# Performance work log

Hardware: AMD Instinct MI355X
Metric: run time of the kernel (lower is better)

The kernel has to match this reference:

```python
import jax, jax.numpy as jnp
import numpy as np

N_ENT = 50000
N_REL = 500
IN_DIM = 128
OUT_DIM = 128
N_EDGES = 500000
LRELU_SLOPE = 0.01  # torch F.leaky_relu default


def setup_inputs() -> dict:
    key = jax.random.key(0)
    ks = jax.random.split(key, 8)
    # triplets [3, E]: row0=src entity, row1=relation, row2=dst entity.
    # Ensure every entity appears as a source so no 0/0 in the edge-softmax division.
    src_extra = jax.random.randint(ks[0], (N_EDGES - N_ENT,), 0, N_ENT)
    src = jnp.concatenate([jnp.arange(N_ENT), src_extra])
    rel = jax.random.randint(ks[1], (N_EDGES,), 0, N_REL)
    dst = jax.random.randint(ks[2], (N_EDGES,), 0, N_ENT)
    triplets = jnp.stack([src, rel, dst]).astype(jnp.int64)
    ent_embed = jax.random.normal(ks[3], (N_ENT, IN_DIM), dtype=jnp.float32)
    rel_embed = jax.random.normal(ks[4], (N_REL, IN_DIM), dtype=jnp.float32)
    adj = jax.random.randint(ks[5], (2, N_EDGES), 0, N_ENT).astype(jnp.int64)  # unused by forward
    # Xavier-normal (gain=1.414) init for the two linear layers, like the torch module.
    std_a = 1.414 * np.sqrt(2.0 / (3 * IN_DIM + OUT_DIM))
    std_a2 = 1.414 * np.sqrt(2.0 / (OUT_DIM + 1))
    W_a = jax.random.normal(ks[6], (3 * IN_DIM, OUT_DIM), dtype=jnp.float32) * std_a
    b_a = jnp.zeros((OUT_DIM,), dtype=jnp.float32)
    W_a2 = jax.random.normal(ks[7], (OUT_DIM, 1), dtype=jnp.float32) * std_a2
    b_a2 = jnp.zeros((1,), dtype=jnp.float32)
    return {"triplets": triplets, "ent_embed": ent_embed, "rel_embed": rel_embed,
            "adj": adj, "W_a": W_a, "b_a": b_a, "W_a2": W_a2, "b_a2": b_a2}


def reference(triplets, ent_embed, rel_embed, adj, W_a, b_a, W_a2, b_a2):
    src, rel, dst = triplets[0], triplets[1], triplets[2]
    n_ent = ent_embed.shape[0]
    # Gather + concat: [E, 3*in_dim]
    h = jnp.concatenate([ent_embed[src], rel_embed[rel], ent_embed[dst]], axis=1)
    c = h @ W_a + b_a                                   # [E, out_dim]
    b = jax.nn.leaky_relu(c @ W_a2 + b_a2, LRELU_SLOPE)  # [E, 1]
    e_b = jnp.exp(b)                                    # [E, 1]
    # Sparse edge-softmax grouped by source node (sparse.sum over dst dim).
    denom = jax.ops.segment_sum(e_b, src, num_segments=n_ent)        # [N, 1]
    numer = jax.ops.segment_sum(e_b * c, src, num_segments=n_ent)    # [N, out_dim]
    out = numer / denom
    return jax.nn.elu(out)  # concat=True branch
```

## Files before the change

kernel.cpp:

```cpp
#include <hip/hip_runtime.h>

#define DIM 128

typedef __attribute__((ext_vector_type(8))) short bf16x8;
typedef __attribute__((ext_vector_type(4))) float f32x4;

__device__ inline unsigned short to_bf16(float f) {
    unsigned u = __float_as_uint(f);
    u = (u + 0x7FFFu + ((u >> 16) & 1u)) >> 16;
    return (unsigned short)u;
}
__device__ inline unsigned pack_bf16(float lo, float hi) {
    return (unsigned)to_bf16(lo) | ((unsigned)to_bf16(hi) << 16);
}
__device__ inline float unpack_lo(unsigned v) { return __uint_as_float(v << 16); }
__device__ inline float unpack_hi(unsigned v) { return __uint_as_float(v & 0xFFFF0000u); }

__global__ void wprep_kernel(const float* __restrict__ W_a, unsigned short* __restrict__ Wt,
                             int* __restrict__ counts, int n) {
    const int c = blockIdx.x;
    const int k = threadIdx.x;
    const int srow = (c < 128) ? k : (256 + k);
    const int scol = (c < 128) ? c : (c - 128);
    Wt[c * DIM + k] = to_bf16(W_a[srow * DIM + scol]);
    for (int i = blockIdx.x * 128 + k; i < n; i += 256 * 128) counts[i] = 0;
}

__global__ __launch_bounds__(512) void gemm_kernel(
        const float* __restrict__ ent, const unsigned short* __restrict__ Wt,
        const float* __restrict__ b_a, const float* __restrict__ Wa2,
        unsigned* __restrict__ P1h, unsigned* __restrict__ P3h,
        float* __restrict__ q1, float* __restrict__ q3, int NE) {
    __shared__ unsigned smem[8320];
    const int b = blockIdx.x;
    const int half = b & 1;
    const int mrow = (b >> 1) * 128;
    const int t = threadIdx.x;
    const int wv = t >> 6;
    const int lane = t & 63;
    const int g = lane >> 4, m = lane & 15;

    const unsigned short* Wh = Wt + half * 128 * DIM;
    #pragma unroll
    for (int i = 0; i < 4; ++i) {
        const int ci  = i * 8 + wv;
        const int row = ci * 4 + (lane >> 4);
        const int dw0 = (lane & 15) * 4;
        const int sdw = dw0 ^ ((row & 7) << 2);
        const uint4 v = *(const uint4*)(Wh + row * DIM + sdw * 2);
        *(uint4*)&smem[ci * 256 + lane * 4] = v;
    }

    const int rowA = min(mrow + wv * 16 + m, NE - 1);
    const float* arow = ent + (size_t)rowA * DIM;
    bf16x8 afrag[4];
    #pragma unroll
    for (int kk = 0; kk < 4; ++kk) {
        const float4 u0 = *(const float4*)(arow + kk * 32 + g * 8);
        const float4 u1 = *(const float4*)(arow + kk * 32 + g * 8 + 4);
        bf16x8 a;
        a[0] = (short)to_bf16(u0.x); a[1] = (short)to_bf16(u0.y);
        a[2] = (short)to_bf16(u0.z); a[3] = (short)to_bf16(u0.w);
        a[4] = (short)to_bf16(u1.x); a[5] = (short)to_bf16(u1.y);
        a[6] = (short)to_bf16(u1.z); a[7] = (short)to_bf16(u1.w);
        afrag[kk] = a;
    }
    __syncthreads();

    f32x4 acc[8];
    #pragma unroll
    for (int ct = 0; ct < 8; ++ct) acc[ct] = (f32x4){0.f, 0.f, 0.f, 0.f};
    #pragma unroll
    for (int kk = 0; kk < 4; ++kk) {
        #pragma unroll
        for (int ct = 0; ct < 8; ++ct) {
            const int dw = (kk * 16 + g * 4) ^ ((m & 7) << 2);
            const bf16x8 bb = *(const bf16x8*)&smem[(ct * 16 + m) * 64 + dw];
            acc[ct] = __builtin_amdgcn_mfma_f32_16x16x32_bf16(afrag[kk], bb, acc[ct], 0, 0, 0);
        }
    }
    __syncthreads();

    unsigned* __restrict__ Ph = half ? P3h : P1h;
    float*    __restrict__ qo = half ? q3  : q1;
    unsigned short* lds16 = (unsigned short*)smem;

    float qp[4] = {0.f, 0.f, 0.f, 0.f};
    #pragma unroll
    for (int ct = 0; ct < 8; ++ct) {
        const int c = ct * 16 + m;
        const float bias = half ? 0.0f : b_a[c];
        const float wa2  = Wa2[c];
        #pragma unroll
        for (int r = 0; r < 4; ++r) {
            const float v = acc[ct][r] + bias;
            qp[r] += v * wa2;
            lds16[(wv * 16 + g * 4 + r) * 130 + c] = to_bf16(v);
        }
    }
    #pragma unroll
    for (int r = 0; r < 4; ++r) {
        float v = qp[r];
        #pragma unroll
        for (int o = 1; o < 16; o <<= 1) v += __shfl_xor(v, o);
        const int row = mrow + wv * 16 + g * 4 + r;
        if (m == 0 && row < NE) qo[row] = v;
    }
    __syncthreads();
    #pragma unroll 4
    for (int i = 0; i < 16; ++i) {
        const int linear = i * 512 + t;
        const int row = linear >> 6, d = linear & 63;
        const int rg = mrow + row;
        if (rg < NE) Ph[(size_t)rg * 64 + d] = smem[row * 65 + d];
    }
}

__global__ __launch_bounds__(256) void histrel_kernel(
        const float* __restrict__ rel, const int* __restrict__ T,
        const float* __restrict__ W_rel, const float* __restrict__ Wa2,
        unsigned* __restrict__ P2h, float* __restrict__ q2,
        int* __restrict__ counts, int NR, int E, int HB) {
    __shared__ float xs[8 * DIM];
    __shared__ float sred[16];
    int b = blockIdx.x;
    const int t = threadIdx.x;

    if (b < HB) {
        for (int e = b * 256 + t; e < E; e += HB * 256)
            atomicAdd(&counts[T[e]], 1);
        return;
    }
    b -= HB;

    const int row0 = b * 8;
    const int half = t >> 7;
    const int tc   = t & 127;
    #pragma unroll
    for (int e = 0; e < 4; ++e) {
        int row = row0 + half * 4 + e;
        xs[(half * 4 + e) * DIM + tc] = (row < NR) ? rel[(size_t)row * DIM + tc] : 0.0f;
    }
    __syncthreads();
    float acc[4] = {0.f, 0.f, 0.f, 0.f};
    #pragma unroll 4
    for (int k = 0; k < DIM; ++k) {
        const float wv = W_rel[k * DIM + tc];
        #pragma unroll
        for (int e = 0; e < 4; ++e) acc[e] += xs[(half * 4 + e) * DIM + k] * wv;
    }
    const float wa2 = Wa2[tc];
    const int lane = t & 63;
    #pragma unroll
    for (int e = 0; e < 4; ++e) {
        float v = acc[e] * wa2;
        #pragma unroll
        for (int o = 32; o > 0; o >>= 1) v += __shfl_down(v, o);
        if (lane == 0) sred[(half * 4 + e) * 2 + ((t >> 6) & 1)] = v;
    }
    __syncthreads();
    #pragma unroll
    for (int e = 0; e < 4; ++e) {
        int row = row0 + half * 4 + e;
        float hi = __shfl_down(acc[e], 1);
        if (row < NR && (tc & 1) == 0)
            P2h[(size_t)row * 64 + (tc >> 1)] = pack_bf16(acc[e], hi);
    }
    if (t < 8) {
        int row = row0 + t;
        if (row < NR) q2[row] = sred[t * 2] + sred[t * 2 + 1];
    }
}

__device__ inline int wave_incl_scan(int v) {
    const int lane = threadIdx.x & 63;
    #pragma unroll
    for (int o = 1; o < 64; o <<= 1) {
        int u = __shfl_up(v, o);
        if (lane >= o) v += u;
    }
    return v;
}

__global__ void scan_bsum_kernel(const int* __restrict__ counts, int* __restrict__ bsum, int n) {
    const int t = threadIdx.x;
    const int base = blockIdx.x * 1024 + t * 4;
    int s = 0;
    #pragma unroll
    for (int j = 0; j < 4; ++j) if (base + j < n) s += counts[base + j];
    #pragma unroll
    for (int o = 32; o > 0; o >>= 1) s += __shfl_down(s, o);
    __shared__ int ws[4];
    if ((t & 63) == 0) ws[t >> 6] = s;
    __syncthreads();
    if (t == 0) bsum[blockIdx.x] = ws[0] + ws[1] + ws[2] + ws[3];
}

__global__ void scan_write_kernel(const int* __restrict__ counts, const int* __restrict__ bsum,
                                  int* __restrict__ offsets, int* __restrict__ cursor,
                                  int n, int total, int nb) {
    __shared__ int s_boff;
    __shared__ int wsum[4], wpre[4];
    const int t = threadIdx.x;
    if (t < 64) {
        int v = (t < nb) ? bsum[t] : 0;
        int incl = wave_incl_scan(v);
        int ex = incl - v;
        int want = __shfl(ex, (int)blockIdx.x);
        if (t == 0) s_boff = want;
    }
    const int base = blockIdx.x * 1024 + t * 4;
    int c[4];
    int s = 0;
    #pragma unroll
    for (int j = 0; j < 4; ++j) {
        c[j] = (base + j < n) ? counts[base + j] : 0;
        s += c[j];
    }
    int incl = wave_incl_scan(s);
    const int wid = t >> 6, lane = t & 63;
    if (lane == 63) wsum[wid] = incl;
    __syncthreads();
    if (t == 0) {
        int run = 0;
        #pragma unroll
        for (int k = 0; k < 4; ++k) { wpre[k] = run; run += wsum[k]; }
    }
    __syncthreads();
    int run = incl - s + wpre[wid] + s_boff;
    #pragma unroll
    for (int j = 0; j < 4; ++j) {
        if (base + j < n) { offsets[base + j] = run; cursor[base + j] = run; run += c[j]; }
    }
    if (base == 0 && blockIdx.x == 0) offsets[n] = total;
}

__global__ void scatter_kernel(const int* __restrict__ T, const float* __restrict__ q1,
                               const float* __restrict__ q2, const float* __restrict__ q3,
                               const float* __restrict__ b_a2, int* __restrict__ cursor,
                               uint2* __restrict__ rdw, int E) {
    const int e = blockIdx.x * blockDim.x + threadIdx.x;
    if (e >= E) return;
    const int s = T[e], r = T[E + e], d = T[2 * E + e];
    float b = q1[s] + q2[r] + q3[d] + b_a2[0];
    b = (b > 0.0f) ? b : 0.01f * b;
    const float wv = __expf(b);
    const int pos = atomicAdd(&cursor[s], 1);
    rdw[pos] = make_uint2(((unsigned)r << 17) | (unsigned)d, __float_as_uint(wv));
}

__global__ void gather_kernel(const int* __restrict__ offsets, const uint2* __restrict__ rdw,
                              const unsigned* __restrict__ P1h, const unsigned* __restrict__ P2h,
                              const unsigned* __restrict__ P3h, float* __restrict__ out, int n) {
    const int node = (blockIdx.x << 2) + (threadIdx.x >> 6);
    if (node >= n) return;
    const int lane = threadIdx.x & 63;
    const int lo = offsets[node], hi = offsets[node + 1];
    float axp[4] = {0.f,0.f,0.f,0.f};
    float ayp[4] = {0.f,0.f,0.f,0.f};
    float wsp[4] = {0.f,0.f,0.f,0.f};
    int i = lo;
    for (; i + 3 < hi; i += 4) {
        uint2 e[4];
        #pragma unroll
        for (int j = 0; j < 4; ++j) e[j] = rdw[i + j];
        unsigned v2[4], v3[4];
        #pragma unroll
        for (int j = 0; j < 4; ++j) {
            v2[j] = P2h[(size_t)(e[j].x >> 17) * 64 + lane];
            v3[j] = P3h[(size_t)(e[j].x & 0x1FFFFu) * 64 + lane];
        }
        #pragma unroll
        for (int j = 0; j < 4; ++j) {
            const float wv = __uint_as_float(e[j].y);
            axp[j] += wv * (unpack_lo(v2[j]) + unpack_lo(v3[j]));
            ayp[j] += wv * (unpack_hi(v2[j]) + unpack_hi(v3[j]));
            wsp[j] += wv;
        }
    }
    for (; i < hi; ++i) {
        const uint2 e0 = rdw[i];
        const unsigned v2a = P2h[(size_t)(e0.x >> 17) * 64 + lane];
        const unsigned v3a = P3h[(size_t)(e0.x & 0x1FFFFu) * 64 + lane];
        const float wv = __uint_as_float(e0.y);
        axp[0] += wv * (unpack_lo(v2a) + unpack_lo(v3a));
        ayp[0] += wv * (unpack_hi(v2a) + unpack_hi(v3a));
        wsp[0] += wv;
    }
    const float ax = (axp[0] + axp[1]) + (axp[2] + axp[3]);
    const float ay = (ayp[0] + ayp[1]) + (ayp[2] + ayp[3]);
    const float inv = 1.0f / ((wsp[0] + wsp[1]) + (wsp[2] + wsp[3]));
    const unsigned p1 = P1h[(size_t)node * 64 + lane];
    float v0 = unpack_lo(p1) + ax * inv;
    float v1 = unpack_hi(p1) + ay * inv;
    v0 = (v0 > 0.0f) ? v0 : (__expf(v0) - 1.0f);
    v1 = (v1 > 0.0f) ? v1 : (__expf(v1) - 1.0f);
    *(float2*)(out + (size_t)node * DIM + (lane << 1)) = make_float2(v0, v1);
}

extern "C" void kernel_launch(void* const* d_in, const int* in_sizes, int n_in,
                              void* d_out, int out_size, void* d_ws, size_t ws_size,
                              hipStream_t stream) {
    const int*   T    = (const int*)d_in[0];
    const float* ent  = (const float*)d_in[1];
    const float* rel  = (const float*)d_in[2];
    const float* W_a  = (const float*)d_in[4];
    const float* b_a  = (const float*)d_in[5];
    const float* W_a2 = (const float*)d_in[6];
    const float* b_a2 = (const float*)d_in[7];
    float* out = (float*)d_out;

    const int E  = in_sizes[0] / 3;
    const int NE = in_sizes[1] / DIM;
    const int NR = in_sizes[2] / DIM;
    const int NB = (NE + 1023) / 1024;
    const int GB = ((NE + 127) / 128) * 2;
    const int HB = 256;
    const int RB = (NR + 7) / 8;

    float* ws = (float*)d_ws;
    size_t off = 0;
    unsigned* P1h = (unsigned*)(ws + off); off += (size_t)NE * 64;
    unsigned* P3h = (unsigned*)(ws + off); off += (size_t)NE * 64;
    unsigned* P2h = (unsigned*)(ws + off); off += (size_t)NR * 64;
    unsigned short* Wt = (unsigned short*)(ws + off); off += 256 * DIM / 2;
    float* q1   = ws + off; off += NE;
    float* q3   = ws + off; off += NE;
    float* q2   = ws + off; off += NR + 64;
    int* counts  = (int*)(ws + off); off += NE;
    int* offsets = (int*)(ws + off); off += NE + 64;
    int* cursor  = (int*)(ws + off); off += NE;
    int* bsum    = (int*)(ws + off); off += 64;
    uint2* rdw   = (uint2*)(ws + off); off += (size_t)E * 2;

    wprep_kernel<<<256, 128, 0, stream>>>(W_a, Wt, counts, NE);

    gemm_kernel<<<GB, 512, 0, stream>>>(ent, Wt, b_a, W_a2, P1h, P3h, q1, q3, NE);

    histrel_kernel<<<HB + RB, 256, 0, stream>>>(rel, T, W_a + 128 * DIM, W_a2,
                                                P2h, q2, counts, NR, E, HB);

    scan_bsum_kernel<<<NB, 256, 0, stream>>>(counts, bsum, NE);
    scan_write_kernel<<<NB, 256, 0, stream>>>(counts, bsum, offsets, cursor, NE, E, NB);

    scatter_kernel<<<(E + 255) / 256, 256, 0, stream>>>(T, q1, q2, q3, b_a2, cursor, rdw, E);

    gather_kernel<<<(NE + 3) / 4, 256, 0, stream>>>(offsets, rdw, P1h, P2h, P3h, out, NE);
}
```

Measured before the change: 118.7 us.

## Merge entity GEMM, histogram, and relation projection into one stage1 kernel

Combines the entity GEMM kernel and the histogram/relation-projection kernel into a single launch with 512-thread blocks. Each GEMM block now computes both the src and dst projections (P1 and P3) for its 128 rows, so the A fragment is loaded and converted once instead of twice. The histogram and relation blocks are resized to 512 threads. The aim is to cut a launch boundary, halve the reads of entity rows, and overlap the histogram atomics with the GEMM, at the cost of twice the LDS per block (about 66KB) and more accumulator registers, which may lower occupancy.

```diff
diff --git a/kernel.cpp b/kernel.cpp
--- a/kernel.cpp
+++ b/kernel.cpp
@@ -26,149 +26,156 @@
     for (int i = blockIdx.x * 128 + k; i < n; i += 256 * 128) counts[i] = 0;
 }
 
-__global__ __launch_bounds__(512) void gemm_kernel(
-        const float* __restrict__ ent, const unsigned short* __restrict__ Wt,
-        const float* __restrict__ b_a, const float* __restrict__ Wa2,
-        unsigned* __restrict__ P1h, unsigned* __restrict__ P3h,
-        float* __restrict__ q1, float* __restrict__ q3, int NE) {
-    __shared__ unsigned smem[8320];
-    const int b = blockIdx.x;
-    const int half = b & 1;
-    const int mrow = (b >> 1) * 128;
-    const int t = threadIdx.x;
-    const int wv = t >> 6;
-    const int lane = t & 63;
-    const int g = lane >> 4, m = lane & 15;
-
-    const unsigned short* Wh = Wt + half * 128 * DIM;
-    #pragma unroll
-    for (int i = 0; i < 4; ++i) {
-        const int ci  = i * 8 + wv;
-        const int row = ci * 4 + (lane >> 4);
-        const int dw0 = (lane & 15) * 4;
-        const int sdw = dw0 ^ ((row & 7) << 2);
-        const uint4 v = *(const uint4*)(Wh + row * DIM + sdw * 2);
-        *(uint4*)&smem[ci * 256 + lane * 4] = v;
-    }
-
-    const int rowA = min(mrow + wv * 16 + m, NE - 1);
-    const float* arow = ent + (size_t)rowA * DIM;
-    bf16x8 afrag[4];
-    #pragma unroll
-    for (int kk = 0; kk < 4; ++kk) {
-        const float4 u0 = *(const float4*)(arow + kk * 32 + g * 8);
-        const float4 u1 = *(const float4*)(arow + kk * 32 + g * 8 + 4);
-        bf16x8 a;
-        a[0] = (short)to_bf16(u0.x); a[1] = (short)to_bf16(u0.y);
-        a[2] = (short)to_bf16(u0.z); a[3] = (short)to_bf16(u0.w);
-        a[4] = (short)to_bf16(u1.x); a[5] = (short)to_bf16(u1.y);
-        a[6] = (short)to_bf16(u1.z); a[7] = (short)to_bf16(u1.w);
-        afrag[kk] = a;
-    }
-    __syncthreads();
-
-    f32x4 acc[8];
-    #pragma unroll
-    for (int ct = 0; ct < 8; ++ct) acc[ct] = (f32x4){0.f, 0.f, 0.f, 0.f};
-    #pragma unroll
-    for (int kk = 0; kk < 4; ++kk) {
-        #pragma unroll
-        for (int ct = 0; ct < 8; ++ct) {
-            const int dw = (kk * 16 + g * 4) ^ ((m & 7) << 2);
-            const bf16x8 bb = *(const bf16x8*)&smem[(ct * 16 + m) * 64 + dw];
-            acc[ct] = __builtin_amdgcn_mfma_f32_16x16x32_bf16(afrag[kk], bb, acc[ct], 0, 0, 0);
-        }
-    }
-    __syncthreads();
-
-    unsigned* __restrict__ Ph = half ? P3h : P1h;
-    float*    __restrict__ qo = half ? q3  : q1;
-    unsigned short* lds16 = (unsigned short*)smem;
-
-    float qp[4] = {0.f, 0.f, 0.f, 0.f};
-    #pragma unroll
-    for (int ct = 0; ct < 8; ++ct) {
-        const int c = ct * 16 + m;
-        const float bias = half ? 0.0f : b_a[c];
-        const float wa2  = Wa2[c];
-        #pragma unroll
-        for (int r = 0; r < 4; ++r) {
-            const float v = acc[ct][r] + bias;
-            qp[r] += v * wa2;
-            lds16[(wv * 16 + g * 4 + r) * 130 + c] = to_bf16(v);
-        }
-    }
-    #pragma unroll
-    for (int r = 0; r < 4; ++r) {
-        float v = qp[r];
-        #pragma unroll
-        for (int o = 1; o < 16; o <<= 1) v += __shfl_xor(v, o);
-        const int row = mrow + wv * 16 + g * 4 + r;
-        if (m == 0 && row < NE) qo[row] = v;
-    }
-    __syncthreads();
-    #pragma unroll 4
-    for (int i = 0; i < 16; ++i) {
-        const int linear = i * 512 + t;
-        const int row = linear >> 6, d = linear & 63;
-        const int rg = mrow + row;
-        if (rg < NE) Ph[(size_t)rg * 64 + d] = smem[row * 65 + d];
-    }
-}
-
-__global__ __launch_bounds__(256) void histrel_kernel(
-        const float* __restrict__ rel, const int* __restrict__ T,
-        const float* __restrict__ W_rel, const float* __restrict__ Wa2,
-        unsigned* __restrict__ P2h, float* __restrict__ q2,
-        int* __restrict__ counts, int NR, int E, int HB) {
-    __shared__ float xs[8 * DIM];
-    __shared__ float sred[16];
+__global__ __launch_bounds__(512, 4) void stage1_kernel(
+        const float* __restrict__ ent, const float* __restrict__ rel,
+        const int* __restrict__ T, const unsigned short* __restrict__ Wt,
+        const float* __restrict__ W_rel, const float* __restrict__ b_a,
+        const float* __restrict__ Wa2,
+        unsigned* __restrict__ P1h, unsigned* __restrict__ P3h, unsigned* __restrict__ P2h,
+        float* __restrict__ q1, float* __restrict__ q3, float* __restrict__ q2,
+        int* __restrict__ counts, int NE, int NR, int E, int GB, int HB, int RB) {
+    __shared__ unsigned smem[16640];
     int b = blockIdx.x;
     const int t = threadIdx.x;
 
+    if (b < GB) {
+        const int mrow = b * 128;
+        const int wv = t >> 6;
+        const int lane = t & 63;
+        const int g = lane >> 4, m = lane & 15;
+
+        #pragma unroll
+        for (int i = 0; i < 8; ++i) {
+            const int ci  = i * 8 + wv;
+            const int row = ci * 4 + (lane >> 4);
+            const int dw0 = (lane & 15) * 4;
+            const int sdw = dw0 ^ ((row & 7) << 2);
+            const uint4 v = *(const uint4*)(Wt + row * DIM + sdw * 2);
+            *(uint4*)&smem[ci * 256 + lane * 4] = v;
+        }
+
+        const int rowA = min(mrow + wv * 16 + m, NE - 1);
+        const float* arow = ent + (size_t)rowA * DIM;
+        bf16x8 afrag[4];
+        #pragma unroll
+        for (int kk = 0; kk < 4; ++kk) {
+            const float4 u0 = *(const float4*)(arow + kk * 32 + g * 8);
+            const float4 u1 = *(const float4*)(arow + kk * 32 + g * 8 + 4);
+            bf16x8 a;
+            a[0] = (short)to_bf16(u0.x); a[1] = (short)to_bf16(u0.y);
+            a[2] = (short)to_bf16(u0.z); a[3] = (short)to_bf16(u0.w);
+            a[4] = (short)to_bf16(u1.x); a[5] = (short)to_bf16(u1.y);
+            a[6] = (short)to_bf16(u1.z); a[7] = (short)to_bf16(u1.w);
+            afrag[kk] = a;
+        }
+        __syncthreads();
+
+        f32x4 acc[2][8];
+        #pragma unroll
+        for (int h = 0; h < 2; ++h)
+            #pragma unroll
+            for (int ct = 0; ct < 8; ++ct) acc[h][ct] = (f32x4){0.f, 0.f, 0.f, 0.f};
+        #pragma unroll
+        for (int kk = 0; kk < 4; ++kk) {
+            #pragma unroll
+            for (int h = 0; h < 2; ++h) {
+                #pragma unroll
+                for (int ct = 0; ct < 8; ++ct) {
+                    const int brow = h * 128 + ct * 16 + m;
+                    const int dw = (kk * 16 + g * 4) ^ ((brow & 7) << 2);
+                    const bf16x8 bb = *(const bf16x8*)&smem[brow * 64 + dw];
+                    acc[h][ct] = __builtin_amdgcn_mfma_f32_16x16x32_bf16(afrag[kk], bb, acc[h][ct], 0, 0, 0);
+                }
+            }
+        }
+        __syncthreads();
+
+        unsigned short* lds16 = (unsigned short*)smem;
+        #pragma unroll
+        for (int h = 0; h < 2; ++h) {
+            float* __restrict__ qo = h ? q3 : q1;
+            float qp[4] = {0.f, 0.f, 0.f, 0.f};
+            #pragma unroll
+            for (int ct = 0; ct < 8; ++ct) {
+                const int c = ct * 16 + m;
+                const float bias = h ? 0.0f : b_a[c];
+                const float wa2  = Wa2[c];
+                #pragma unroll
+                for (int r = 0; r < 4; ++r) {
+                    const float v = acc[h][ct][r] + bias;
+                    qp[r] += v * wa2;
+                    lds16[(h * 128 + wv * 16 + g * 4 + r) * 130 + c] = to_bf16(v);
+                }
+            }
+            #pragma unroll
+            for (int r = 0; r < 4; ++r) {
+                float v = qp[r];
+                #pragma unroll
+                for (int o = 1; o < 16; o <<= 1) v += __shfl_xor(v, o);
+                const int row = mrow + wv * 16 + g * 4 + r;
+                if (m == 0 && row < NE) qo[row] = v;
+            }
+        }
+        __syncthreads();
+        #pragma unroll 4
+        for (int i = 0; i < 32; ++i) {
+            const int linear = i * 512 + t;
+            const int row = linear >> 6, d = linear & 63;
+            const int rg = mrow + (row & 127);
+            unsigned* __restrict__ Ph = (row < 128) ? P1h : P3h;
+            if (rg < NE) Ph[(size_t)rg * 64 + d] = smem[row * 65 + d];
+        }
+        return;
+    }
+    b -= GB;
+
     if (b < HB) {
-        for (int e = b * 256 + t; e < E; e += HB * 256)
+        for (int e = b * 512 + t; e < E; e += HB * 512)
             atomicAdd(&counts[T[e]], 1);
         return;
     }
     b -= HB;
 
-    const int row0 = b * 8;
-    const int half = t >> 7;
-    const int tc   = t & 127;
-    #pragma unroll
-    for (int e = 0; e < 4; ++e) {
-        int row = row0 + half * 4 + e;
-        xs[(half * 4 + e) * DIM + tc] = (row < NR) ? rel[(size_t)row * DIM + tc] : 0.0f;
-    }
-    __syncthreads();
-    float acc[4] = {0.f, 0.f, 0.f, 0.f};
-    #pragma unroll 4
-    for (int k = 0; k < DIM; ++k) {
-        const float wv = W_rel[k * DIM + tc];
-        #pragma unroll
-        for (int e = 0; e < 4; ++e) acc[e] += xs[(half * 4 + e) * DIM + k] * wv;
-    }
-    const float wa2 = Wa2[tc];
-    const int lane = t & 63;
-    #pragma unroll
-    for (int e = 0; e < 4; ++e) {
-        float v = acc[e] * wa2;
-        #pragma unroll
-        for (int o = 32; o > 0; o >>= 1) v += __shfl_down(v, o);
-        if (lane == 0) sred[(half * 4 + e) * 2 + ((t >> 6) & 1)] = v;
-    }
-    __syncthreads();
-    #pragma unroll
-    for (int e = 0; e < 4; ++e) {
-        int row = row0 + half * 4 + e;
-        float hi = __shfl_down(acc[e], 1);
-        if (row < NR && (tc & 1) == 0)
-            P2h[(size_t)row * 64 + (tc >> 1)] = pack_bf16(acc[e], hi);
-    }
-    if (t < 8) {
-        int row = row0 + t;
-        if (row < NR) q2[row] = sred[t * 2] + sred[t * 2 + 1];
+    {
+        float* xs   = (float*)smem;
+        float* sred = (float*)(smem + 2048);
+        const int row0 = b * 16;
+        const int qr = t >> 7;
+        const int tc = t & 127;
+        #pragma unroll
+        for (int e = 0; e < 4; ++e) {
+            int row = row0 + qr * 4 + e;
+            xs[(qr * 4 + e) * DIM + tc] = (row < NR) ? rel[(size_t)row * DIM + tc] : 0.0f;
+        }
+        __syncthreads();
+        float acc[4] = {0.f, 0.f, 0.f, 0.f};
+        #pragma unroll 4
+        for (int k = 0; k < DIM; ++k) {
+            const float wv = W_rel[k * DIM + tc];
+            #pragma unroll
+            for (int e = 0; e < 4; ++e) acc[e] += xs[(qr * 4 + e) * DIM + k] * wv;
+        }
+        const float wa2 = Wa2[tc];
+        const int lane = t & 63;
+        #pragma unroll
+        for (int e = 0; e < 4; ++e) {
+            float v = acc[e] * wa2;
+            #pragma unroll
+            for (int o = 32; o > 0; o >>= 1) v += __shfl_down(v, o);
+            if (lane == 0) sred[(qr * 4 + e) * 2 + ((t >> 6) & 1)] = v;
+        }
+        __syncthreads();
+        #pragma unroll
+        for (int e = 0; e < 4; ++e) {
+            int row = row0 + qr * 4 + e;
+            float hi = __shfl_down(acc[e], 1);
+            if (row < NR && (tc & 1) == 0)
+                P2h[(size_t)row * 64 + (tc >> 1)] = pack_bf16(acc[e], hi);
+        }
+        if (t < 16) {
+            int row = row0 + t;
+            if (row < NR) q2[row] = sred[t * 2] + sred[t * 2 + 1];
+        }
     }
 }
 
@@ -314,9 +321,9 @@
     const int NE = in_sizes[1] / DIM;
     const int NR = in_sizes[2] / DIM;
     const int NB = (NE + 1023) / 1024;
-    const int GB = ((NE + 127) / 128) * 2;
-    const int HB = 256;
-    const int RB = (NR + 7) / 8;
+    const int GB = (NE + 127) / 128;
+    const int HB = 128;
+    const int RB = (NR + 15) / 16;
 
     float* ws = (float*)d_ws;
     size_t off = 0;
@@ -335,10 +342,9 @@
 
     wprep_kernel<<<256, 128, 0, stream>>>(W_a, Wt, counts, NE);
 
-    gemm_kernel<<<GB, 512, 0, stream>>>(ent, Wt, b_a, W_a2, P1h, P3h, q1, q3, NE);
-
-    histrel_kernel<<<HB + RB, 256, 0, stream>>>(rel, T, W_a + 128 * DIM, W_a2,
-                                                P2h, q2, counts, NR, E, HB);
+    stage1_kernel<<<GB + HB + RB, 512, 0, stream>>>(
+        ent, rel, T, Wt, W_a + 128 * DIM, b_a, W_a2,
+        P1h, P3h, P2h, q1, q3, q2, counts, NE, NR, E, GB, HB, RB);
 
     scan_bsum_kernel<<<NB, 256, 0, stream>>>(counts, bsum, NE);
     scan_write_kernel<<<NB, 256, 0, stream>>>(counts, bsum, offsets, cursor, NE, E, NB);
```

After: 101.1 us. 14.8% less time.
